# Kernel tuning notes

Hardware: AMD Instinct MI355X
Metric: run time of the kernel (lower is better)

Reference implementation:

```python
import jax, jax.numpy as jnp
import numpy as np

D_IN = 1024
D_OUT = 1024
NUM_HEAD = 16
HEAD_DIM = D_OUT // NUM_HEAD
CTX = 2048


def setup_inputs() -> dict:
    key = jax.random.key(0)
    ks = jax.random.split(key, 7)
    s = 0.02
    x = jax.random.normal(ks[0], (2, CTX, D_IN), dtype=jnp.float32)
    Wq = jax.random.normal(ks[1], (D_IN, D_OUT), dtype=jnp.float32) * s
    Wk = jax.random.normal(ks[2], (D_IN, D_OUT), dtype=jnp.float32) * s
    Wv = jax.random.normal(ks[3], (D_IN, D_OUT), dtype=jnp.float32) * s
    Wo = jax.random.normal(ks[4], (D_OUT, D_OUT), dtype=jnp.float32) * s
    bo = jax.random.normal(ks[5], (D_OUT,), dtype=jnp.float32) * s
    return {"x": x, "Wq": Wq, "Wk": Wk, "Wv": Wv, "Wo": Wo, "bo": bo}


def reference(x, Wq, Wk, Wv, Wo, bo):
    B, T, _ = x.shape
    # QKV projections, split into heads: [B, H, T, hd]
    def split_heads(y):
        return y.reshape(B, T, NUM_HEAD, HEAD_DIM).transpose(0, 2, 1, 3)
    q = split_heads(x @ Wq)
    k = split_heads(x @ Wk)
    v = split_heads(x @ Wv)
    # scaled causal attention scores [B, H, T, T]
    scores = jnp.einsum("bhqd,bhkd->bhqk", q, k) / jnp.sqrt(
        jnp.asarray(HEAD_DIM, dtype=x.dtype))
    causal = jnp.tril(jnp.ones((T, T), dtype=bool))  # mask buffer triu(diag=1) -> keep lower tri
    scores = jnp.where(causal[None, None], scores, jnp.asarray(-jnp.inf, dtype=x.dtype))
    attn = jax.nn.softmax(scores, axis=-1)
    # dropout with droprate=0.0 is identity
    ctx = jnp.einsum("bhqk,bhkd->bhqd", attn, v)
    ctx = ctx.transpose(0, 2, 1, 3).reshape(B, T, D_OUT)
    return ctx @ Wo + bo
```

## Files before the change

kernel.cpp:

```cpp
#include <hip/hip_runtime.h>

typedef __bf16 bf16x8 __attribute__((ext_vector_type(8)));
typedef float f32x4 __attribute__((ext_vector_type(4)));
typedef float f32x16 __attribute__((ext_vector_type(16)));
typedef unsigned int u32x4 __attribute__((ext_vector_type(4)));

__device__ inline unsigned short f2bf(float f) {
    unsigned int x = __builtin_bit_cast(unsigned int, f);
    x += 0x7fff + ((x >> 16) & 1);
    return (unsigned short)(x >> 16);
}

__device__ __forceinline__ void gl_lds16(const unsigned short* g, unsigned short* l)
{
    __builtin_amdgcn_global_load_lds(
        (const __attribute__((address_space(1))) void*)g,
        (__attribute__((address_space(3))) void*)l, 16, 0, 0);
}

__global__ __launch_bounds__(256)
void prep(const float* __restrict__ x, unsigned short* __restrict__ xb,
          const float* __restrict__ Wq, const float* __restrict__ Wk,
          const float* __restrict__ Wv, unsigned short* __restrict__ wT)
{
    __shared__ unsigned short T[64][72];
    if (blockIdx.x < 2048) {
        const size_t i = ((size_t)blockIdx.x * 256 + threadIdx.x) * 8;
        float4 a = *reinterpret_cast<const float4*>(x + i);
        float4 b = *reinterpret_cast<const float4*>(x + i + 4);
        unsigned short t[8] = { f2bf(a.x), f2bf(a.y), f2bf(a.z), f2bf(a.w),
                                f2bf(b.x), f2bf(b.y), f2bf(b.z), f2bf(b.w) };
        *reinterpret_cast<uint4*>(xb + i) = *reinterpret_cast<uint4*>(t);
        return;
    }
    const int blk = blockIdx.x - 2048;
    const int z = blk >> 8, within = blk & 255;
    const float* W = (z == 0) ? Wq : (z == 1) ? Wk : Wv;
    unsigned short* dstBase = wT + (size_t)z * 1024 * 1024;
    const int k0 = (within >> 4) * 64, n0 = (within & 15) * 64;
    const int r = threadIdx.x >> 2, c0 = (threadIdx.x & 3) * 16;
    const float* src = W + (size_t)(k0 + r) * 1024 + n0 + c0;
    #pragma unroll
    for (int j = 0; j < 16; j += 4) {
        float4 f = *reinterpret_cast<const float4*>(src + j);
        T[r][c0 + j]     = f2bf(f.x);
        T[r][c0 + j + 1] = f2bf(f.y);
        T[r][c0 + j + 2] = f2bf(f.z);
        T[r][c0 + j + 3] = f2bf(f.w);
    }
    __syncthreads();
    unsigned short* dst = dstBase + (size_t)(n0 + r) * 1024 + k0 + c0;
    #pragma unroll
    for (int h = 0; h < 2; ++h) {
        unsigned short t8[8];
        #pragma unroll
        for (int j = 0; j < 8; ++j) t8[j] = T[c0 + h * 8 + j][r];
        *reinterpret_cast<uint4*>(dst + h * 8) = *reinterpret_cast<uint4*>(t8);
    }
}

__global__ __launch_bounds__(256)
void wconv(const float* __restrict__ W, unsigned short* __restrict__ wT)
{
    __shared__ unsigned short T[64][72];
    const int k0 = blockIdx.y * 64, n0 = blockIdx.x * 64;
    const int r = threadIdx.x >> 2, c0 = (threadIdx.x & 3) * 16;
    const float* src = W + (size_t)(k0 + r) * 1024 + n0 + c0;
    #pragma unroll
    for (int j = 0; j < 16; j += 4) {
        float4 f = *reinterpret_cast<const float4*>(src + j);
        T[r][c0 + j]     = f2bf(f.x);
        T[r][c0 + j + 1] = f2bf(f.y);
        T[r][c0 + j + 2] = f2bf(f.z);
        T[r][c0 + j + 3] = f2bf(f.w);
    }
    __syncthreads();
    unsigned short* dst = wT + (size_t)(n0 + r) * 1024 + k0 + c0;
    #pragma unroll
    for (int h = 0; h < 2; ++h) {
        unsigned short t8[8];
        #pragma unroll
        for (int j = 0; j < 8; ++j) t8[j] = T[c0 + h * 8 + j][r];
        *reinterpret_cast<uint4*>(dst + h * 8) = *reinterpret_cast<uint4*>(t8);
    }
}

template <int MODE>
__global__ __launch_bounds__(256)
void gemm128(const unsigned short* __restrict__ A,
             const unsigned short* __restrict__ BT,
             void* __restrict__ C0, void* __restrict__ C1,
             void* __restrict__ C2, const float* __restrict__ bias)
{
    __shared__ unsigned short As[128 * 32];
    __shared__ unsigned short Bs[128 * 32];

    const int tid = threadIdx.x;
    const int wave = tid >> 6, lane = tid & 63, quad = lane >> 4, l16 = lane & 15;
    const int wm = wave >> 1, wn = wave & 1;

    const int nwx = gridDim.x;
    const int L   = (int)(blockIdx.y * nwx + blockIdx.x);
    const int cpx = (int)(nwx * gridDim.y) >> 3;
    const int sw  = (L & 7) * cpx + (L >> 3);
    const int mBase = (sw / nwx) * 128, nBase = (sw % nwx) * 128;

    f32x4 acc[4][4] = {};

    const int srow = lane >> 2, sko = (lane & 3) * 8;

    for (int kb = 0; kb < 1024; kb += 32) {
        __syncthreads();
        #pragma unroll
        for (int j = 0; j < 2; ++j) {
            const int seg = wave * 2 + j;
            gl_lds16(A  + (size_t)(mBase + seg * 16 + srow) * 1024 + kb + sko,
                     As + seg * 512);
            gl_lds16(BT + (size_t)(nBase + seg * 16 + srow) * 1024 + kb + sko,
                     Bs + seg * 512);
        }
        __syncthreads();

        bf16x8 af[4], bf[4];
        #pragma unroll
        for (int t = 0; t < 4; ++t) {
            af[t] = *reinterpret_cast<const bf16x8*>(&As[(wm * 64 + t * 16 + l16) * 32 + quad * 8]);
            bf[t] = *reinterpret_cast<const bf16x8*>(&Bs[(wn * 64 + t * 16 + l16) * 32 + quad * 8]);
        }
        #pragma unroll
        for (int ti = 0; ti < 4; ++ti)
            #pragma unroll
            for (int tj = 0; tj < 4; ++tj)
                acc[ti][tj] = __builtin_amdgcn_mfma_f32_16x16x32_bf16(
                    af[ti], bf[tj], acc[ti][tj], 0, 0, 0);
    }

    #pragma unroll
    for (int ti = 0; ti < 4; ++ti) {
        const int row0 = mBase + wm * 64 + ti * 16 + quad * 4;
        #pragma unroll
        for (int tj = 0; tj < 4; ++tj) {
            const int col = nBase + wn * 64 + tj * 16 + l16;
            if constexpr (MODE == 0) {
                if (col < 1024) {
                    unsigned short* qb = (unsigned short*)C0;
                    #pragma unroll
                    for (int i = 0; i < 4; ++i)
                        qb[(size_t)(row0 + i) * 1024 + col] = f2bf(acc[ti][tj][i]);
                } else if (col < 2048) {
                    unsigned short* kb = (unsigned short*)C1;
                    #pragma unroll
                    for (int i = 0; i < 4; ++i)
                        kb[(size_t)(row0 + i) * 1024 + col - 1024] = f2bf(acc[ti][tj][i]);
                } else {
                    unsigned short* vT = (unsigned short*)C2;
                    unsigned short t4[4] = { f2bf(acc[ti][tj][0]), f2bf(acc[ti][tj][1]),
                                             f2bf(acc[ti][tj][2]), f2bf(acc[ti][tj][3]) };
                    *reinterpret_cast<uint2*>(&vT[(size_t)(col - 2048) * 4096 + row0]) =
                        *reinterpret_cast<uint2*>(t4);
                }
            } else {
                float* out = (float*)C0;
                const float ba = bias[col];
                #pragma unroll
                for (int i = 0; i < 4; ++i)
                    out[(size_t)(row0 + i) * 1024 + col] = acc[ti][tj][i] + ba;
            }
        }
    }
}

__global__ __launch_bounds__(256, 2)
void attn11(const unsigned short* __restrict__ q,
            const unsigned short* __restrict__ k,
            const unsigned short* __restrict__ vT,
            unsigned short* __restrict__ ctx)
{
    __shared__ unsigned short Ks[3][64 * 64];
    __shared__ unsigned short Vs[3][64 * 64];
    __shared__ float Lt[8 * 64];

    const int tid  = threadIdx.x;
    const int wave = tid >> 6, lane = tid & 63;
    const int q32 = lane & 31, hi = lane >> 5;
    const int slice = wave & 1;
    const int ks    = wave >> 1;
    const int j  = blockIdx.x;
    const int bh = blockIdx.y;
    const int b = bh >> 4, h = bh & 15;
    const int tokBase = b * 2048;
    const int colBase = h * 64;
    const int qtA = 31 - j, qtB = j;
    const int qloA = qtA * 64 + slice * 32;
    const int qloB = qtB * 64 + slice * 32;

    bf16x8 aqA[4], aqB[4];
    {
        const unsigned short* ra = q + (size_t)(tokBase + qloA + q32) * 1024 + colBase + hi * 8;
        const unsigned short* rb = q + (size_t)(tokBase + qloB + q32) * 1024 + colBase + hi * 8;
        #pragma unroll
        for (int c = 0; c < 4; ++c) {
            aqA[c] = *reinterpret_cast<const bf16x8*>(ra + c * 16);
            aqB[c] = *reinterpret_cast<const bf16x8*>(rb + c * 16);
        }
    }
    #pragma unroll
    for (int c = 0; c < 4; ++c)
        asm volatile("" :: "v"(aqA[c]), "v"(aqB[c]));

    f32x16 oA[2] = {}, oB[2] = {};
    float lsA = 0.0f, lsB = 0.0f;

    const int s0 = (wave * 2 + 0) * 64 + lane;
    const int s1 = (wave * 2 + 1) * 64 + lane;
    const int r0 = s0 >> 3, sw0 = (s0 & 7) ^ (r0 & 7);
    const int r1 = s1 >> 3, sw1 = (s1 & 7) ^ (r1 & 7);
    const size_t kOff0 = (size_t)r0 * 1024 + colBase + sw0 * 8;
    const size_t kOff1 = (size_t)r1 * 1024 + colBase + sw1 * 8;
    const size_t vOff0 = (size_t)(colBase + r0) * 4096 + sw0 * 8;
    const size_t vOff1 = (size_t)(colBase + r1) * 4096 + sw1 * 8;

    auto stage = [&](int tok0, int buf) {
        gl_lds16(k  + (size_t)tok0 * 1024 + kOff0, &Ks[buf][(wave * 2 + 0) * 512]);
        gl_lds16(k  + (size_t)tok0 * 1024 + kOff1, &Ks[buf][(wave * 2 + 1) * 512]);
        gl_lds16(vT + vOff0 + tok0,                &Vs[buf][(wave * 2 + 0) * 512]);
        gl_lds16(vT + vOff1 + tok0,                &Vs[buf][(wave * 2 + 1) * 512]);
    };

    bf16x8 ak[4];
    bf16x8 bv[2][2];

    const int nkt = qtA + 1;
    stage(tokBase, 0);
    stage(tokBase + 64, 1);

    int cur = 0;
    const int krowK = ks * 32 + q32;
    for (int kt = 0; kt < nkt; ++kt) {
        if (kt + 1 < nkt) asm volatile("s_waitcnt vmcnt(4)" ::: "memory");
        else              asm volatile("s_waitcnt vmcnt(0)" ::: "memory");
        __builtin_amdgcn_s_barrier();
        asm volatile("" ::: "memory");

        const int stg = (cur == 0) ? 2 : cur - 1;
        if (kt + 2 < nkt)
            stage(tokBase + (kt + 2) * 64, stg);

        const unsigned short* KsB = Ks[cur];
        const unsigned short* VsB = Vs[cur];
        #pragma unroll
        for (int c = 0; c < 4; ++c) {
            const int u = c * 2 + hi;
            ak[c] = *reinterpret_cast<const bf16x8*>(
                &KsB[krowK * 64 + ((u ^ (krowK & 7)) * 8)]);
        }
        #pragma unroll
        for (int kc = 0; kc < 2; ++kc)
            #pragma unroll
            for (int dh = 0; dh < 2; ++dh) {
                const int vrow = dh * 32 + q32;
                const int u = ks * 4 + kc * 2 + hi;
                bv[kc][dh] = *reinterpret_cast<const bf16x8*>(
                    &VsB[vrow * 64 + ((u ^ (vrow & 7)) * 8)]);
            }

        const int klo = kt * 64 + ks * 32;
        const bool dB = (klo <= qloB + 31);
        const bool dA = (klo <= qloA + 31);

        if (dB) {
            f32x16 scA = (f32x16)0.0f, scB = (f32x16)0.0f;
            #pragma unroll
            for (int c = 0; c < 4; ++c) {
                scA = __builtin_amdgcn_mfma_f32_32x32x16_bf16(ak[c], aqA[c], scA, 0, 0, 0);
                scB = __builtin_amdgcn_mfma_f32_32x32x16_bf16(ak[c], aqB[c], scB, 0, 0, 0);
            }
            float pA[16], pB[16];
            #pragma unroll
            for (int r = 0; r < 16; ++r) {
                pA[r] = __expf(scA[r] * 0.125f);
                pB[r] = __expf(scB[r] * 0.125f);
            }
            if (klo + 31 > qloB) {
                #pragma unroll
                for (int r = 0; r < 16; ++r) {
                    const int krow = (r & 3) + 8 * (r >> 2) + 4 * hi;
                    if (klo + krow > qloB + q32) pB[r] = 0.0f;
                }
            }
            #pragma unroll
            for (int r = 0; r < 16; ++r) { lsA += pA[r]; lsB += pB[r]; }
            unsigned int pkA[8], pkB[8];
            #pragma unroll
            for (int i = 0; i < 8; ++i) {
                asm("v_cvt_pk_bf16_f32 %0, %1, %2"
                    : "=v"(pkA[i]) : "v"(pA[2 * i]), "v"(pA[2 * i + 1]));
                asm("v_cvt_pk_bf16_f32 %0, %1, %2"
                    : "=v"(pkB[i]) : "v"(pB[2 * i]), "v"(pB[2 * i + 1]));
            }
            #pragma unroll
            for (int kc = 0; kc < 2; ++kc) {
                unsigned int xa0 = pkA[kc * 4 + 0], ya0 = pkA[kc * 4 + 2];
                unsigned int xa1 = pkA[kc * 4 + 1], ya1 = pkA[kc * 4 + 3];
                unsigned int xb0 = pkB[kc * 4 + 0], yb0 = pkB[kc * 4 + 2];
                unsigned int xb1 = pkB[kc * 4 + 1], yb1 = pkB[kc * 4 + 3];
                asm("v_permlane32_swap_b32 %0, %1" : "+v"(xa0), "+v"(ya0));
                asm("v_permlane32_swap_b32 %0, %1" : "+v"(xa1), "+v"(ya1));
                asm("v_permlane32_swap_b32 %0, %1" : "+v"(xb0), "+v"(yb0));
                asm("v_permlane32_swap_b32 %0, %1" : "+v"(xb1), "+v"(yb1));
                const u32x4 wa = { xa0, xa1, ya0, ya1 };
                const u32x4 wb = { xb0, xb1, yb0, yb1 };
                const bf16x8 paA = __builtin_bit_cast(bf16x8, wa);
                const bf16x8 paB = __builtin_bit_cast(bf16x8, wb);
                #pragma unroll
                for (int dh = 0; dh < 2; ++dh) {
                    oA[dh] = __builtin_amdgcn_mfma_f32_32x32x16_bf16(paA, bv[kc][dh], oA[dh], 0, 0, 0);
                    oB[dh] = __builtin_amdgcn_mfma_f32_32x32x16_bf16(paB, bv[kc][dh], oB[dh], 0, 0, 0);
                }
            }
        } else if (dA) {
            f32x16 sc = (f32x16)0.0f;
            #pragma unroll
            for (int c = 0; c < 4; ++c)
                sc = __builtin_amdgcn_mfma_f32_32x32x16_bf16(ak[c], aqA[c], sc, 0, 0, 0);
            float p[16];
            #pragma unroll
            for (int r = 0; r < 16; ++r) p[r] = __expf(sc[r] * 0.125f);
            if (klo + 31 > qloA) {
                #pragma unroll
                for (int r = 0; r < 16; ++r) {
                    const int krow = (r & 3) + 8 * (r >> 2) + 4 * hi;
                    if (klo + krow > qloA + q32) p[r] = 0.0f;
                }
            }
            #pragma unroll
            for (int r = 0; r < 16; ++r) lsA += p[r];
            unsigned int pk[8];
            #pragma unroll
            for (int i = 0; i < 8; ++i)
                asm("v_cvt_pk_bf16_f32 %0, %1, %2"
                    : "=v"(pk[i]) : "v"(p[2 * i]), "v"(p[2 * i + 1]));
            #pragma unroll
            for (int kc = 0; kc < 2; ++kc) {
                unsigned int x0 = pk[kc * 4 + 0], y0 = pk[kc * 4 + 2];
                unsigned int x1 = pk[kc * 4 + 1], y1 = pk[kc * 4 + 3];
                asm("v_permlane32_swap_b32 %0, %1" : "+v"(x0), "+v"(y0));
                asm("v_permlane32_swap_b32 %0, %1" : "+v"(x1), "+v"(y1));
                const u32x4 wv = { x0, x1, y0, y1 };
                const bf16x8 pa = __builtin_bit_cast(bf16x8, wv);
                #pragma unroll
                for (int dh = 0; dh < 2; ++dh)
                    oA[dh] = __builtin_amdgcn_mfma_f32_32x32x16_bf16(pa, bv[kc][dh], oA[dh], 0, 0, 0);
            }
        }
        cur = (cur == 2) ? 0 : cur + 1;
    }

    float* Obuf = reinterpret_cast<float*>(&Ks[0][0]);

    __syncthreads();
    Lt[(wave * 2 + 0) * 64 + lane] = lsA;
    Lt[(wave * 2 + 1) * 64 + lane] = lsB;

    auto writePartial = [&](const f32x16 (&o)[2]) {
        float* slot = Obuf + slice * 2048;
        #pragma unroll
        for (int r = 0; r < 16; ++r) {
            const int row = (r & 3) + 8 * (r >> 2) + 4 * hi;
            #pragma unroll
            for (int dh = 0; dh < 2; ++dh)
                slot[row * 64 + dh * 32 + q32] = o[dh][r];
        }
    };
    auto finalize = [&](int t, int qt, const f32x16 (&o)[2]) {
        const float lf = Lt[(slice * 2 + t) * 64 + q32]
                       + Lt[(slice * 2 + t) * 64 + 32 + q32]
                       + Lt[((slice + 2) * 2 + t) * 64 + q32]
                       + Lt[((slice + 2) * 2 + t) * 64 + 32 + q32];
        const float inv = 1.0f / lf;
        const float* slot = Obuf + slice * 2048;
        #pragma unroll
        for (int r = 0; r < 16; ++r) {
            const int row = (r & 3) + 8 * (r >> 2) + 4 * hi;
            const float invr = __shfl(inv, row);
            const size_t gr = (size_t)(tokBase + qt * 64 + slice * 32 + row) * 1024 + colBase;
            #pragma unroll
            for (int dh = 0; dh < 2; ++dh)
                ctx[gr + dh * 32 + q32] =
                    f2bf((o[dh][r] + slot[row * 64 + dh * 32 + q32]) * invr);
        }
    };

    if (ks == 1) writePartial(oA);
    __syncthreads();
    if (ks == 0) finalize(0, qtA, oA);
    __syncthreads();
    if (ks == 0) writePartial(oB);
    __syncthreads();
    if (ks == 1) finalize(1, qtB, oB);
}

extern "C" void kernel_launch(void* const* d_in, const int* in_sizes, int n_in,
                              void* d_out, int out_size, void* d_ws, size_t ws_size,
                              hipStream_t stream)
{
    const float* x  = (const float*)d_in[0];
    const float* Wq = (const float*)d_in[1];
    const float* Wk = (const float*)d_in[2];
    const float* Wv = (const float*)d_in[3];
    const float* Wo = (const float*)d_in[4];
    const float* bo = (const float*)d_in[5];
    float* out = (float*)d_out;

    unsigned short* xb     = (unsigned short*)d_ws;
    unsigned short* qb     = xb + (size_t)4096 * 1024;
    unsigned short* kb     = qb + (size_t)4096 * 1024;
    unsigned short* vT     = kb + (size_t)4096 * 1024;
    unsigned short* ctx    = xb;
    unsigned short* wqkvT  = (unsigned short*)d_out;
    unsigned short* woT    = kb;

    prep<<<2816, 256, 0, stream>>>(x, xb, Wq, Wk, Wv, wqkvT);

    gemm128<0><<<dim3(24, 32), 256, 0, stream>>>(xb, wqkvT, qb, kb, vT, nullptr);

    attn11<<<dim3(16, 32), 256, 0, stream>>>(qb, kb, vT, ctx);

    wconv<<<dim3(16, 16), 256, 0, stream>>>(Wo, woT);

    gemm128<2><<<dim3(8, 32), 256, 0, stream>>>(ctx, woT, out, nullptr, nullptr, bo);
}
```

Baseline: 184.2 us.

## Replace QKV GEMM with double-buffered 128x192 tile kernel using swizzled LDS

Adds a new QKV projection kernel with 512 threads, 128x192 output tiles, K-step 64, double-buffered LDS staging with an XOR swizzle, and a single barrier per iteration so the next tile's loads overlap the current MFMAs. The aim is to cut barrier stalls and LDS bank conflicts and to give 512 blocks instead of 768. The block-index swizzle is also removed from the remaining output GEMM, which may hurt L2 locality there.

```diff
diff --git a/kernel.cpp b/kernel.cpp
--- a/kernel.cpp
+++ b/kernel.cpp
@@ -85,6 +85,100 @@
     }
 }
 
+__global__ __launch_bounds__(512, 4)
+void gemm8p(const unsigned short* __restrict__ A,
+            const unsigned short* __restrict__ BT,
+            unsigned short* __restrict__ qb,
+            unsigned short* __restrict__ kb,
+            unsigned short* __restrict__ vT)
+{
+    __shared__ unsigned short As[2][128 * 64];
+    __shared__ unsigned short Bs[2][192 * 64];
+
+    const int tid  = threadIdx.x;
+    const int wave = tid >> 6, lane = tid & 63;
+    const int quad = lane >> 4, l16 = lane & 15;
+    const int wm = wave >> 2, wn = wave & 3;
+    const int mBase = blockIdx.y * 128, nBase = blockIdx.x * 192;
+
+    f32x4 acc[4][3] = {};
+
+    const int arow = tid >> 3;
+    const int u8   = (tid & 7) ^ (arow & 7);
+    const int rx   = l16 & 7;
+
+    auto stage = [&](int kb0, int buf) {
+        #pragma unroll
+        for (int i = 0; i < 2; ++i)
+            gl_lds16(A + (size_t)(mBase + i * 64 + arow) * 1024 + kb0 + u8 * 8,
+                     &As[buf][(i * 512 + wave * 64) * 8]);
+        #pragma unroll
+        for (int i = 0; i < 3; ++i)
+            gl_lds16(BT + (size_t)(nBase + i * 64 + arow) * 1024 + kb0 + u8 * 8,
+                     &Bs[buf][(i * 512 + wave * 64) * 8]);
+    };
+
+    stage(0, 0);
+    __syncthreads();
+
+    for (int t = 0; t < 16; ++t) {
+        const int buf = t & 1;
+        if (t + 1 < 16)
+            stage((t + 1) * 64, buf ^ 1);
+
+        #pragma unroll
+        for (int kh = 0; kh < 2; ++kh) {
+            bf16x8 af[4], bf[3];
+            #pragma unroll
+            for (int mr = 0; mr < 4; ++mr) {
+                const int row = wm * 64 + mr * 16 + l16;
+                af[mr] = *reinterpret_cast<const bf16x8*>(
+                    &As[buf][row * 64 + (((kh * 4 + quad) ^ rx) * 8)]);
+            }
+            #pragma unroll
+            for (int nr = 0; nr < 3; ++nr) {
+                const int row = wn * 48 + nr * 16 + l16;
+                bf[nr] = *reinterpret_cast<const bf16x8*>(
+                    &Bs[buf][row * 64 + (((kh * 4 + quad) ^ rx) * 8)]);
+            }
+            #pragma unroll
+            for (int mr = 0; mr < 4; ++mr)
+                #pragma unroll
+                for (int nr = 0; nr < 3; ++nr)
+                    acc[mr][nr] = __builtin_amdgcn_mfma_f32_16x16x32_bf16(
+                        af[mr], bf[nr], acc[mr][nr], 0, 0, 0);
+        }
+
+        if (t + 1 < 16) {
+            asm volatile("s_waitcnt vmcnt(0)" ::: "memory");
+            __builtin_amdgcn_s_barrier();
+        }
+    }
+
+    #pragma unroll
+    for (int mr = 0; mr < 4; ++mr) {
+        const int row0 = mBase + wm * 64 + mr * 16 + quad * 4;
+        #pragma unroll
+        for (int nr = 0; nr < 3; ++nr) {
+            const int col = nBase + wn * 48 + nr * 16 + l16;
+            if (col < 1024) {
+                #pragma unroll
+                for (int i = 0; i < 4; ++i)
+                    qb[(size_t)(row0 + i) * 1024 + col] = f2bf(acc[mr][nr][i]);
+            } else if (col < 2048) {
+                #pragma unroll
+                for (int i = 0; i < 4; ++i)
+                    kb[(size_t)(row0 + i) * 1024 + col - 1024] = f2bf(acc[mr][nr][i]);
+            } else {
+                unsigned short t4[4] = { f2bf(acc[mr][nr][0]), f2bf(acc[mr][nr][1]),
+                                         f2bf(acc[mr][nr][2]), f2bf(acc[mr][nr][3]) };
+                *reinterpret_cast<uint2*>(&vT[(size_t)(col - 2048) * 4096 + row0]) =
+                    *reinterpret_cast<uint2*>(t4);
+            }
+        }
+    }
+}
+
 template <int MODE>
 __global__ __launch_bounds__(256)
 void gemm128(const unsigned short* __restrict__ A,
@@ -98,12 +192,7 @@
     const int tid = threadIdx.x;
     const int wave = tid >> 6, lane = tid & 63, quad = lane >> 4, l16 = lane & 15;
     const int wm = wave >> 1, wn = wave & 1;
-
-    const int nwx = gridDim.x;
-    const int L   = (int)(blockIdx.y * nwx + blockIdx.x);
-    const int cpx = (int)(nwx * gridDim.y) >> 3;
-    const int sw  = (L & 7) * cpx + (L >> 3);
-    const int mBase = (sw / nwx) * 128, nBase = (sw % nwx) * 128;
+    const int mBase = blockIdx.y * 128, nBase = blockIdx.x * 128;
 
     f32x4 acc[4][4] = {};
 
@@ -141,31 +230,11 @@
         #pragma unroll
         for (int tj = 0; tj < 4; ++tj) {
             const int col = nBase + wn * 64 + tj * 16 + l16;
-            if constexpr (MODE == 0) {
-                if (col < 1024) {
-                    unsigned short* qb = (unsigned short*)C0;
-                    #pragma unroll
-                    for (int i = 0; i < 4; ++i)
-                        qb[(size_t)(row0 + i) * 1024 + col] = f2bf(acc[ti][tj][i]);
-                } else if (col < 2048) {
-                    unsigned short* kb = (unsigned short*)C1;
-                    #pragma unroll
-                    for (int i = 0; i < 4; ++i)
-                        kb[(size_t)(row0 + i) * 1024 + col - 1024] = f2bf(acc[ti][tj][i]);
-                } else {
-                    unsigned short* vT = (unsigned short*)C2;
-                    unsigned short t4[4] = { f2bf(acc[ti][tj][0]), f2bf(acc[ti][tj][1]),
-                                             f2bf(acc[ti][tj][2]), f2bf(acc[ti][tj][3]) };
-                    *reinterpret_cast<uint2*>(&vT[(size_t)(col - 2048) * 4096 + row0]) =
-                        *reinterpret_cast<uint2*>(t4);
-                }
-            } else {
-                float* out = (float*)C0;
-                const float ba = bias[col];
-                #pragma unroll
-                for (int i = 0; i < 4; ++i)
-                    out[(size_t)(row0 + i) * 1024 + col] = acc[ti][tj][i] + ba;
-            }
+            float* out = (float*)C0;
+            const float ba = bias[col];
+            #pragma unroll
+            for (int i = 0; i < 4; ++i)
+                out[(size_t)(row0 + i) * 1024 + col] = acc[ti][tj][i] + ba;
         }
     }
 }
@@ -422,7 +491,7 @@
 
     prep<<<2816, 256, 0, stream>>>(x, xb, Wq, Wk, Wv, wqkvT);
 
-    gemm128<0><<<dim3(24, 32), 256, 0, stream>>>(xb, wqkvT, qb, kb, vT, nullptr);
+    gemm8p<<<dim3(16, 32), 512, 0, stream>>>(xb, wqkvT, qb, kb, vT);
 
     attn11<<<dim3(16, 32), 256, 0, stream>>>(qb, kb, vT, ctx);
 
```

Result: faster. 179.3 us (-2.7%).
